# Performance work log

Hardware: AMD Instinct MI355X
Metric: run time of the kernel (lower is better)

Reference implementation:

```python
import jax, jax.numpy as jnp
import numpy as np

EMBED_DIM = 768
M, C = 8192, 4096
NEG_SAMPLES = 2   # args.neg_sample
CL_TEMP = 1.0
P_INF = 1000.0
EPS = 1e-8


def exp_map0(x, curv):
    # Lorentz exponential map at the origin (space components only, MERU-style).
    rc_xnorm = jnp.sqrt(curv) * jnp.linalg.norm(x, axis=-1, keepdims=True)
    return jnp.sinh(rc_xnorm) * x / jnp.maximum(rc_xnorm, EPS)


def pairwise_dist(x, y, curv):
    # x: (m, d) space components, y: (c, d); Lorentz geodesic distance.
    x_time = jnp.sqrt(1.0 / curv + jnp.sum(x * x, axis=-1))   # (m,)
    y_time = jnp.sqrt(1.0 / curv + jnp.sum(y * y, axis=-1))   # (c,)
    inner = x @ y.T - x_time[:, None] * y_time[None, :]        # Lorentz inner product (m, c)
    cd = jnp.maximum(-curv * inner, 1.0 + EPS)
    return jnp.arccosh(cd) / jnp.sqrt(curv)


def setup_inputs() -> dict:
    key = jax.random.key(0)
    k1, k2, k3 = jax.random.split(key, 3)
    return {
        "text_embeddings": jax.random.normal(k1, (M, EMBED_DIM), dtype=jnp.float32),
        "label_embeddings": jax.random.normal(k2, (C, EMBED_DIM), dtype=jnp.float32),
        "target_labels": jax.random.randint(k3, (M,), 0, C),
        "curv_log": jnp.float32(np.log(1.0)),                      # curv param (log-space)
        "text_alpha_log": jnp.float32(np.log(EMBED_DIM ** -0.5)),  # text_alpha (log-space)
        "label_alpha_log": jnp.float32(np.log(EMBED_DIM ** -0.5)), # label_alpha (log-space)
    }


def reference(text_embeddings, label_embeddings, target_labels, curv_log, text_alpha_log, label_alpha_log):
    curv = jnp.exp(curv_log)
    te = text_embeddings * jnp.exp(text_alpha_log)
    le = label_embeddings * jnp.exp(label_alpha_log)
    text_hyp = exp_map0(te, curv)
    label_hyp = exp_map0(le, curv)
    dist = pairwise_dist(text_hyp, label_hyp, curv)        # (m, c)
    m = dist.shape[0]
    rows = jnp.arange(m)
    # hard-negative mining: mask out the positive label, take k smallest distances
    masked = dist.at[rows, target_labels].set(P_INF)
    neg_minus_dist, _ = jax.lax.top_k(-masked, NEG_SAMPLES)  # (m, k) = -dist of hardest negatives
    neg_scores = neg_minus_dist / CL_TEMP                     # -dist / temp
    pos_score = -dist[rows, target_labels] / CL_TEMP          # (m,)
    denom = jnp.exp(pos_score) + jnp.sum(jnp.exp(neg_scores), axis=-1)
    loss = jnp.log(denom) - pos_score                         # = -log(exp(pos)/denom)
    return loss                                               # (m,) per-sample losses
```

## Files before the change

kernel.cpp:

```cpp
#include <hip/hip_runtime.h>
#include <hip/hip_bf16.h>
#include <math.h>

#define MM 8192
#define CC 4096
#define DD 768
#define EPSF 1e-8f

#define BM 256
#define BN 256
#define BK 64
#define TPB 512
#define NKT (DD / BK)
#define NROWT (MM / BM)
#define NCOLT (CC / BN)

#define XB_OFF 0
#define YB_OFF (MM * DD * 2)
#define FW_OFF (YB_OFF + CC * DD * 2)
#define S_T 0
#define T_T (MM)
#define S_L (2 * MM)
#define T_L (2 * MM + CC)
#define CA_T (2 * MM + 2 * CC)
#define POS  (CA_T + MM)
#define PART (POS + MM)

typedef __attribute__((ext_vector_type(8))) short short8;
typedef __attribute__((ext_vector_type(4))) unsigned short u16x4;
typedef __attribute__((ext_vector_type(4))) float f32x4;

__device__ inline unsigned short f2bf(float f) {
    unsigned int u = __float_as_uint(f);
    u += 0x7FFF + ((u >> 16) & 1);
    return (unsigned short)(u >> 16);
}

__device__ inline void gll16(const void* g, void* l) {
    __builtin_amdgcn_global_load_lds(
        (const __attribute__((address_space(1))) void*)(uintptr_t)g,
        (__attribute__((address_space(3))) void*)(unsigned)(uintptr_t)l,
        16, 0, 0);
}

#define BAR() do { __builtin_amdgcn_sched_barrier(0); __builtin_amdgcn_s_barrier(); __builtin_amdgcn_sched_barrier(0); } while (0)
#define VM8 asm volatile("s_waitcnt vmcnt(8)" ::: "memory")
#define VM4 asm volatile("s_waitcnt vmcnt(4)" ::: "memory")
#define VM0 asm volatile("s_waitcnt vmcnt(0)" ::: "memory")
#define NOPS ((void)0)

#define DSR(dst, base, off) \
    asm volatile("ds_read_b128 %0, %1 offset:%c2" : "=v"(dst) : "v"(base), "n"(off))

#define MFMA_B(a, b, c) __builtin_amdgcn_mfma_f32_16x16x32_bf16((a), (b), (c), 0, 0, 0)

__global__ void prep_conv_kernel(const float* __restrict__ X, const float* __restrict__ Y,
                                 const float* curv_log, const float* ta_log, const float* la_log,
                                 char* __restrict__ wsb) {
    unsigned short* Xb = (unsigned short*)(wsb + XB_OFF);
    unsigned short* Yb = (unsigned short*)(wsb + YB_OFF);
    float* fws = (float*)(wsb + FW_OFF);
    int wid = threadIdx.x >> 6, lane = threadIdx.x & 63;
    int row = blockIdx.x * 4 + wid;
    float curv = __expf(curv_log[0]);
    const float* src; unsigned short* dst; float alpha; int idx; int is_text;
    if (row < MM) {
        src = X + (size_t)row * DD; dst = Xb + (size_t)row * DD;
        alpha = __expf(ta_log[0]); idx = row; is_text = 1;
    } else {
        int r = row - MM;
        src = Y + (size_t)r * DD; dst = Yb + (size_t)r * DD;
        alpha = __expf(la_log[0]); idx = r; is_text = 0;
    }
    float n2 = 0.f;
    #pragma unroll
    for (int j = 0; j < 3; ++j) {
        float4 v = *(const float4*)(src + lane * 4 + 256 * j);
        n2 += v.x * v.x + v.y * v.y + v.z * v.z + v.w * v.w;
        u16x4 o; o[0] = f2bf(v.x); o[1] = f2bf(v.y); o[2] = f2bf(v.z); o[3] = f2bf(v.w);
        *(u16x4*)(dst + lane * 4 + 256 * j) = o;
    }
    #pragma unroll
    for (int m = 32; m; m >>= 1) n2 += __shfl_xor(n2, m);
    if (lane == 0) {
        float r = sqrtf(curv) * alpha * sqrtf(n2);
        float s = alpha * sinhf(r) / fmaxf(r, EPSF);
        float tt = sqrtf(1.0f / curv + s * s * n2);
        if (is_text) {
            fws[S_T + idx] = s; fws[T_T + idx] = tt; fws[CA_T + idx] = tt / s;
        } else {
            fws[S_L + idx] = s; fws[T_L + idx] = tt;
        }
    }
}

__global__ void pos_kernel(const float* __restrict__ X, const float* __restrict__ Y,
                           const int* __restrict__ tgt, const float* curv_log,
                           char* __restrict__ wsb) {
    float* fws = (float*)(wsb + FW_OFF);
    int wid = threadIdx.x >> 6, lane = threadIdx.x & 63;
    int row = blockIdx.x * 4 + wid;
    if (row >= MM) return;
    float curv = __expf(curv_log[0]);
    int t = tgt[row];
    const float* xr = X + (size_t)row * DD;
    const float* yr = Y + (size_t)t * DD;
    float dot = 0.f;
    #pragma unroll
    for (int k = 0; k < DD / 64; ++k) dot += xr[lane + 64 * k] * yr[lane + 64 * k];
    #pragma unroll
    for (int m = 32; m; m >>= 1) dot += __shfl_xor(dot, m);
    if (lane == 0) {
        float inner = fws[S_T + row] * fws[S_L + t] * dot - fws[T_T + row] * fws[T_L + t];
        float cd = fmaxf(-curv * inner, 1.0f + EPSF);
        float d = __logf(cd + sqrtf(cd * cd - 1.0f)) * rsqrtf(curv);
        fws[POS + row] = d;
    }
}

__global__ __launch_bounds__(TPB, 2) void main_kernel(
    const int* __restrict__ tgt, char* __restrict__ wsb)
{
    __shared__ unsigned short Ald[4 * 8192];
    __shared__ unsigned short Bld[4 * 8192];
    __shared__ float red[256][4][2];

    const unsigned short* Xb = (const unsigned short*)(wsb + XB_OFF);
    const unsigned short* Yb = (const unsigned short*)(wsb + YB_OFF);
    float* fws = (float*)(wsb + FW_OFF);

    int tid = threadIdx.x;
    int lane = tid & 63, wid = tid >> 6;
    int wr = wid >> 2, wc = wid & 3;
    int l15 = lane & 15, rgrp = lane >> 4;

    int bid = blockIdx.x;
    int pos = bid >> 3;
    int coltile = pos >> 2;
    int rowpanel = (bid & 7) * 4 + (pos & 3);
    int rowbase = rowpanel * BM;
    int colbase = coltile * BN;

    int ko_src = ((tid & 3) ^ ((tid >> 3) & 3)) * 8;
    const unsigned short* xk = Xb + (size_t)(rowbase + (tid >> 2)) * DD + ko_src;
    const unsigned short* yk = Yb + (size_t)(colbase + (tid >> 2)) * DD + ko_src;
    unsigned short* adst = Ald + tid * 8;
    unsigned short* bdst = Bld + tid * 8;

#define STG_A(OFF, RG) do { gll16(xk + (OFF), adst + (RG) * 8192); \
                            gll16(xk + (size_t)128 * DD + (OFF), adst + (RG) * 8192 + 4096); } while (0)
#define STG_B(OFF, RG) do { gll16(yk + (OFF), bdst + (RG) * 8192); \
                            gll16(yk + (size_t)128 * DD + (OFF), bdst + (RG) * 8192 + 4096); } while (0)

    unsigned a_base = (unsigned)(uintptr_t)(&Ald[0]) + (wr * 128 + l15) * 64
                      + ((rgrp * 16) ^ (((l15 >> 1) & 3) << 4));
    unsigned b_base = (unsigned)(uintptr_t)(&Bld[0]) + (wc * 64 + l15) * 64
                      + ((rgrp * 16) ^ (((l15 >> 1) & 3) << 4));

    f32x4 acc[8][4];
    #pragma unroll
    for (int a = 0; a < 8; ++a)
        #pragma unroll
        for (int b = 0; b < 4; ++b)
            acc[a][b] = (f32x4){0.f, 0.f, 0.f, 0.f};

    short8 af[4], bf[4];

#define MF16(AO) do { \
    acc[(AO)+0][0] = MFMA_B(af[0], bf[0], acc[(AO)+0][0]); \
    acc[(AO)+0][1] = MFMA_B(af[0], bf[1], acc[(AO)+0][1]); \
    acc[(AO)+0][2] = MFMA_B(af[0], bf[2], acc[(AO)+0][2]); \
    acc[(AO)+0][3] = MFMA_B(af[0], bf[3], acc[(AO)+0][3]); \
    acc[(AO)+1][0] = MFMA_B(af[1], bf[0], acc[(AO)+1][0]); \
    acc[(AO)+1][1] = MFMA_B(af[1], bf[1], acc[(AO)+1][1]); \
    acc[(AO)+1][2] = MFMA_B(af[1], bf[2], acc[(AO)+1][2]); \
    acc[(AO)+1][3] = MFMA_B(af[1], bf[3], acc[(AO)+1][3]); \
    acc[(AO)+2][0] = MFMA_B(af[2], bf[0], acc[(AO)+2][0]); \
    acc[(AO)+2][1] = MFMA_B(af[2], bf[1], acc[(AO)+2][1]); \
    acc[(AO)+2][2] = MFMA_B(af[2], bf[2], acc[(AO)+2][2]); \
    acc[(AO)+2][3] = MFMA_B(af[2], bf[3], acc[(AO)+2][3]); \
    acc[(AO)+3][0] = MFMA_B(af[3], bf[0], acc[(AO)+3][0]); \
    acc[(AO)+3][1] = MFMA_B(af[3], bf[1], acc[(AO)+3][1]); \
    acc[(AO)+3][2] = MFMA_B(af[3], bf[2], acc[(AO)+3][2]); \
    acc[(AO)+3][3] = MFMA_B(af[3], bf[3], acc[(AO)+3][3]); \
} while (0)

#define PHASE(RG, MH, AO, STG, W) do { \
    if ((MH) == 0) { \
        DSR(bf[0], b_base, (RG) * 16384 + 0); \
        DSR(bf[1], b_base, (RG) * 16384 + 1024); \
        DSR(bf[2], b_base, (RG) * 16384 + 2048); \
        DSR(bf[3], b_base, (RG) * 16384 + 3072); \
    } \
    DSR(af[0], a_base, (RG) * 16384 + ((MH) * 4 + 0) * 1024); \
    DSR(af[1], a_base, (RG) * 16384 + ((MH) * 4 + 1) * 1024); \
    DSR(af[2], a_base, (RG) * 16384 + ((MH) * 4 + 2) * 1024); \
    DSR(af[3], a_base, (RG) * 16384 + ((MH) * 4 + 3) * 1024); \
    STG; \
    W; \
    BAR(); \
    asm volatile("s_waitcnt lgkmcnt(0)" ::: "memory"); \
    __builtin_amdgcn_sched_barrier(0); \
    __builtin_amdgcn_s_setprio(1); \
    MF16(AO); \
    __builtin_amdgcn_s_setprio(0); \
    BAR(); \
} while (0)

    STG_A(0, 0);  STG_B(0, 0);
    STG_A(32, 1); STG_B(32, 1);
    STG_A(64, 2); STG_B(64, 2);
    VM8;
    BAR();

    #pragma unroll 1
    for (int kp = 0; kp < 5; ++kp) {
        PHASE(0, 0, 0, STG_A(96, 3),  NOPS);
        PHASE(0, 1, 4, STG_B(96, 3),  VM8);
        PHASE(1, 0, 0, STG_A(128, 0), NOPS);
        PHASE(1, 1, 4, STG_B(128, 0), VM8);
        PHASE(2, 0, 0, STG_A(160, 1), NOPS);
        PHASE(2, 1, 4, STG_B(160, 1), VM8);
        PHASE(3, 0, 0, STG_A(192, 2), NOPS);
        PHASE(3, 1, 4, STG_B(192, 2), VM8);
        xk += 128; yk += 128;
    }
    PHASE(0, 0, 0, STG_A(96, 3), NOPS);
    PHASE(0, 1, 4, STG_B(96, 3), VM8);
    PHASE(1, 0, 0, NOPS, NOPS);
    PHASE(1, 1, 4, NOPS, VM4);
    PHASE(2, 0, 0, NOPS, NOPS);
    PHASE(2, 1, 4, NOPS, VM0);
    PHASE(3, 0, 0, NOPS, NOPS);
    PHASE(3, 1, 4, NOPS, NOPS);

    int colb = colbase + wc * 64 + l15;
    float sbv[4], tbv[4];
    #pragma unroll
    for (int nf = 0; nf < 4; ++nf) { sbv[nf] = fws[S_L + colb + nf * 16]; tbv[nf] = fws[T_L + colb + nf * 16]; }

    float m1[32], m2[32];
    #pragma unroll
    for (int mf = 0; mf < 8; ++mf) {
        int rw = rowbase + wr * 128 + mf * 16 + rgrp * 4;
        #pragma unroll
        for (int j = 0; j < 4; ++j) {
            float ca = fws[CA_T + rw + j];
            int tgj = tgt[rw + j];
            float a = -3.4e38f, b = -3.4e38f;
            #pragma unroll
            for (int nf = 0; nf < 4; ++nf) {
                float u = sbv[nf] * acc[mf][nf][j] - ca * tbv[nf];
                if (colb + nf * 16 == tgj) u = -3.4e38f;
                float n1 = fmaxf(a, u);
                b = fmaxf(b, fminf(a, u));
                a = n1;
            }
            m1[mf * 4 + j] = a; m2[mf * 4 + j] = b;
        }
    }
    #pragma unroll
    for (int mask = 1; mask <= 8; mask <<= 1)
        #pragma unroll
        for (int i = 0; i < 32; ++i) {
            float o1 = __shfl_xor(m1[i], mask);
            float o2 = __shfl_xor(m2[i], mask);
            float n1 = fmaxf(m1[i], o1);
            m2[i] = fmaxf(fminf(m1[i], o1), fmaxf(m2[i], o2));
            m1[i] = n1;
        }
    if (l15 == 0) {
        #pragma unroll
        for (int mf = 0; mf < 8; ++mf)
            #pragma unroll
            for (int j = 0; j < 4; ++j) {
                int rl = wr * 128 + mf * 16 + rgrp * 4 + j;
                red[rl][wc][0] = m1[mf * 4 + j];
                red[rl][wc][1] = m2[mf * 4 + j];
            }
    }
    __syncthreads();
    if (tid < 256) {
        float p1 = -3.4e38f, p2 = -3.4e38f;
        #pragma unroll
        for (int g = 0; g < 4; ++g) {
            float a1 = red[tid][g][0], a2 = red[tid][g][1];
            float n1 = fmaxf(p1, a1);
            p2 = fmaxf(fminf(p1, a1), fmaxf(p2, a2));
            p1 = n1;
        }
        int row = rowbase + tid;
        fws[PART + ((size_t)row * NCOLT + coltile) * 2 + 0] = p1;
        fws[PART + ((size_t)row * NCOLT + coltile) * 2 + 1] = p2;
    }
}

__global__ void final_kernel(const char* __restrict__ wsb, const float* __restrict__ curv_log,
                             float* __restrict__ out) {
    const float* fws = (const float*)(wsb + FW_OFF);
    int row = blockIdx.x * 256 + threadIdx.x;
    if (row >= MM) return;
    float curv = __expf(curv_log[0]);
    float rsc = rsqrtf(curv);
    const float* p = fws + PART + (size_t)row * (NCOLT * 2);
    float p1 = -3.4e38f, p2 = -3.4e38f;
    #pragma unroll
    for (int s = 0; s < NCOLT; ++s) {
        float a1 = p[s * 2], a2 = p[s * 2 + 1];
        float n1 = fmaxf(p1, a1);
        p2 = fmaxf(fminf(p1, a1), fmaxf(p2, a2));
        p1 = n1;
    }
    float sa = fws[S_T + row];
    float i1 = sa * p1, i2 = sa * p2;
    float cd1 = fmaxf(-curv * i1, 1.0f + EPSF);
    float d1 = __logf(cd1 + sqrtf(cd1 * cd1 - 1.0f)) * rsc;
    float cd2 = fmaxf(-curv * i2, 1.0f + EPSF);
    float d2 = __logf(cd2 + sqrtf(cd2 * cd2 - 1.0f)) * rsc;
    float dp = fws[POS + row];
    float denom = __expf(-dp) + __expf(-d1) + __expf(-d2);
    out[row] = __logf(denom) + dp;
}

extern "C" void kernel_launch(void* const* d_in, const int* in_sizes, int n_in,
                              void* d_out, int out_size, void* d_ws, size_t ws_size,
                              hipStream_t stream) {
    const float* X = (const float*)d_in[0];
    const float* Y = (const float*)d_in[1];
    const int* tgt = (const int*)d_in[2];
    const float* curv_log = (const float*)d_in[3];
    const float* ta_log = (const float*)d_in[4];
    const float* la_log = (const float*)d_in[5];
    char* wsb = (char*)d_ws;
    float* out = (float*)d_out;

    prep_conv_kernel<<<(MM + CC) / 4, 256, 0, stream>>>(X, Y, curv_log, ta_log, la_log, wsb);
    pos_kernel<<<MM / 4, 256, 0, stream>>>(X, Y, tgt, curv_log, wsb);
    main_kernel<<<NROWT * NCOLT, TPB, 0, stream>>>(tgt, wsb);
    final_kernel<<<MM / 256, 256, 0, stream>>>(wsb, curv_log, out);
}
```

Measured before the change: 89.17 us.

## Double-buffer LDS fragment reads to overlap ds_read with MFMA in GEMM main loop

Splits the A and B register fragments into ping-pong buffers so each phase issues the LDS reads for the next sub-tile before running the MFMAs on the current one. It waits only partially on lgkmcnt and adjusts the vmcnt waits to match. It also drops the min-blocks-per-CU launch bound so the compiler can use more registers for the extra fragment buffers. This costs more VGPRs, which may lower occupancy, and relies on the hand-tuned waitcnt values staying correct.

```diff
diff --git a/kernel.cpp b/kernel.cpp
--- a/kernel.cpp
+++ b/kernel.cpp
@@ -45,6 +45,7 @@
 
 #define BAR() do { __builtin_amdgcn_sched_barrier(0); __builtin_amdgcn_s_barrier(); __builtin_amdgcn_sched_barrier(0); } while (0)
 #define VM8 asm volatile("s_waitcnt vmcnt(8)" ::: "memory")
+#define VM6 asm volatile("s_waitcnt vmcnt(6)" ::: "memory")
 #define VM4 asm volatile("s_waitcnt vmcnt(4)" ::: "memory")
 #define VM0 asm volatile("s_waitcnt vmcnt(0)" ::: "memory")
 #define NOPS ((void)0)
@@ -118,7 +119,7 @@
     }
 }
 
-__global__ __launch_bounds__(TPB, 2) void main_kernel(
+__global__ __launch_bounds__(TPB) void main_kernel(
     const int* __restrict__ tgt, char* __restrict__ wsb)
 {
     __shared__ unsigned short Ald[4 * 8192];
@@ -164,45 +165,47 @@
         for (int b = 0; b < 4; ++b)
             acc[a][b] = (f32x4){0.f, 0.f, 0.f, 0.f};
 
-    short8 af[4], bf[4];
-
-#define MF16(AO) do { \
-    acc[(AO)+0][0] = MFMA_B(af[0], bf[0], acc[(AO)+0][0]); \
-    acc[(AO)+0][1] = MFMA_B(af[0], bf[1], acc[(AO)+0][1]); \
-    acc[(AO)+0][2] = MFMA_B(af[0], bf[2], acc[(AO)+0][2]); \
-    acc[(AO)+0][3] = MFMA_B(af[0], bf[3], acc[(AO)+0][3]); \
-    acc[(AO)+1][0] = MFMA_B(af[1], bf[0], acc[(AO)+1][0]); \
-    acc[(AO)+1][1] = MFMA_B(af[1], bf[1], acc[(AO)+1][1]); \
-    acc[(AO)+1][2] = MFMA_B(af[1], bf[2], acc[(AO)+1][2]); \
-    acc[(AO)+1][3] = MFMA_B(af[1], bf[3], acc[(AO)+1][3]); \
-    acc[(AO)+2][0] = MFMA_B(af[2], bf[0], acc[(AO)+2][0]); \
-    acc[(AO)+2][1] = MFMA_B(af[2], bf[1], acc[(AO)+2][1]); \
-    acc[(AO)+2][2] = MFMA_B(af[2], bf[2], acc[(AO)+2][2]); \
-    acc[(AO)+2][3] = MFMA_B(af[2], bf[3], acc[(AO)+2][3]); \
-    acc[(AO)+3][0] = MFMA_B(af[3], bf[0], acc[(AO)+3][0]); \
-    acc[(AO)+3][1] = MFMA_B(af[3], bf[1], acc[(AO)+3][1]); \
-    acc[(AO)+3][2] = MFMA_B(af[3], bf[2], acc[(AO)+3][2]); \
-    acc[(AO)+3][3] = MFMA_B(af[3], bf[3], acc[(AO)+3][3]); \
+    short8 afE[4], afO[4], bf0[4], bf1[4];
+
+#define LDA(S, RG, MH) do { \
+    DSR(S[0], a_base, (RG) * 16384 + ((MH) * 4 + 0) * 1024); \
+    DSR(S[1], a_base, (RG) * 16384 + ((MH) * 4 + 1) * 1024); \
+    DSR(S[2], a_base, (RG) * 16384 + ((MH) * 4 + 2) * 1024); \
+    DSR(S[3], a_base, (RG) * 16384 + ((MH) * 4 + 3) * 1024); } while (0)
+#define LDB(S, RG) do { \
+    DSR(S[0], b_base, (RG) * 16384 + 0); \
+    DSR(S[1], b_base, (RG) * 16384 + 1024); \
+    DSR(S[2], b_base, (RG) * 16384 + 2048); \
+    DSR(S[3], b_base, (RG) * 16384 + 3072); } while (0)
+
+#define MF16(AF, BF, AO) do { \
+    acc[(AO)+0][0] = MFMA_B(AF[0], BF[0], acc[(AO)+0][0]); \
+    acc[(AO)+0][1] = MFMA_B(AF[0], BF[1], acc[(AO)+0][1]); \
+    acc[(AO)+0][2] = MFMA_B(AF[0], BF[2], acc[(AO)+0][2]); \
+    acc[(AO)+0][3] = MFMA_B(AF[0], BF[3], acc[(AO)+0][3]); \
+    acc[(AO)+1][0] = MFMA_B(AF[1], BF[0], acc[(AO)+1][0]); \
+    acc[(AO)+1][1] = MFMA_B(AF[1], BF[1], acc[(AO)+1][1]); \
+    acc[(AO)+1][2] = MFMA_B(AF[1], BF[2], acc[(AO)+1][2]); \
+    acc[(AO)+1][3] = MFMA_B(AF[1], BF[3], acc[(AO)+1][3]); \
+    acc[(AO)+2][0] = MFMA_B(AF[2], BF[0], acc[(AO)+2][0]); \
+    acc[(AO)+2][1] = MFMA_B(AF[2], BF[1], acc[(AO)+2][1]); \
+    acc[(AO)+2][2] = MFMA_B(AF[2], BF[2], acc[(AO)+2][2]); \
+    acc[(AO)+2][3] = MFMA_B(AF[2], BF[3], acc[(AO)+2][3]); \
+    acc[(AO)+3][0] = MFMA_B(AF[3], BF[0], acc[(AO)+3][0]); \
+    acc[(AO)+3][1] = MFMA_B(AF[3], BF[1], acc[(AO)+3][1]); \
+    acc[(AO)+3][2] = MFMA_B(AF[3], BF[2], acc[(AO)+3][2]); \
+    acc[(AO)+3][3] = MFMA_B(AF[3], BF[3], acc[(AO)+3][3]); \
 } while (0)
 
-#define PHASE(RG, MH, AO, STG, W) do { \
-    if ((MH) == 0) { \
-        DSR(bf[0], b_base, (RG) * 16384 + 0); \
-        DSR(bf[1], b_base, (RG) * 16384 + 1024); \
-        DSR(bf[2], b_base, (RG) * 16384 + 2048); \
-        DSR(bf[3], b_base, (RG) * 16384 + 3072); \
-    } \
-    DSR(af[0], a_base, (RG) * 16384 + ((MH) * 4 + 0) * 1024); \
-    DSR(af[1], a_base, (RG) * 16384 + ((MH) * 4 + 1) * 1024); \
-    DSR(af[2], a_base, (RG) * 16384 + ((MH) * 4 + 2) * 1024); \
-    DSR(af[3], a_base, (RG) * 16384 + ((MH) * 4 + 3) * 1024); \
+#define PH(LD, STG, W, LGN, MF) do { \
+    LD; \
     STG; \
     W; \
     BAR(); \
-    asm volatile("s_waitcnt lgkmcnt(0)" ::: "memory"); \
+    asm volatile("s_waitcnt lgkmcnt(" #LGN ")" ::: "memory"); \
     __builtin_amdgcn_sched_barrier(0); \
     __builtin_amdgcn_s_setprio(1); \
-    MF16(AO); \
+    MF; \
     __builtin_amdgcn_s_setprio(0); \
     BAR(); \
 } while (0)
@@ -212,27 +215,28 @@
     STG_A(64, 2); STG_B(64, 2);
     VM8;
     BAR();
+    LDB(bf0, 0); LDA(afE, 0, 0);
 
     #pragma unroll 1
     for (int kp = 0; kp < 5; ++kp) {
-        PHASE(0, 0, 0, STG_A(96, 3),  NOPS);
-        PHASE(0, 1, 4, STG_B(96, 3),  VM8);
-        PHASE(1, 0, 0, STG_A(128, 0), NOPS);
-        PHASE(1, 1, 4, STG_B(128, 0), VM8);
-        PHASE(2, 0, 0, STG_A(160, 1), NOPS);
-        PHASE(2, 1, 4, STG_B(160, 1), VM8);
-        PHASE(3, 0, 0, STG_A(192, 2), NOPS);
-        PHASE(3, 1, 4, STG_B(192, 2), VM8);
+        PH(LDA(afO, 0, 1),               STG_A(96, 3),  VM6, 4, MF16(afE, bf0, 0));
+        PH(LDB(bf1, 1); LDA(afE, 1, 0),  STG_B(96, 3),  VM6, 8, MF16(afO, bf0, 4));
+        PH(LDA(afO, 1, 1),               STG_A(128, 0), VM6, 4, MF16(afE, bf1, 0));
+        PH(LDB(bf0, 2); LDA(afE, 2, 0),  STG_B(128, 0), VM6, 8, MF16(afO, bf1, 4));
+        PH(LDA(afO, 2, 1),               STG_A(160, 1), VM6, 4, MF16(afE, bf0, 0));
+        PH(LDB(bf1, 3); LDA(afE, 3, 0),  STG_B(160, 1), VM6, 8, MF16(afO, bf0, 4));
+        PH(LDA(afO, 3, 1),               STG_A(192, 2), VM6, 4, MF16(afE, bf1, 0));
+        PH(LDB(bf0, 0); LDA(afE, 0, 0),  STG_B(192, 2), VM6, 8, MF16(afO, bf1, 4));
         xk += 128; yk += 128;
     }
-    PHASE(0, 0, 0, STG_A(96, 3), NOPS);
-    PHASE(0, 1, 4, STG_B(96, 3), VM8);
-    PHASE(1, 0, 0, NOPS, NOPS);
-    PHASE(1, 1, 4, NOPS, VM4);
-    PHASE(2, 0, 0, NOPS, NOPS);
-    PHASE(2, 1, 4, NOPS, VM0);
-    PHASE(3, 0, 0, NOPS, NOPS);
-    PHASE(3, 1, 4, NOPS, NOPS);
+    PH(LDA(afO, 0, 1),               STG_A(96, 3), VM6, 4, MF16(afE, bf0, 0));
+    PH(LDB(bf1, 1); LDA(afE, 1, 0),  STG_B(96, 3), VM6, 8, MF16(afO, bf0, 4));
+    PH(LDA(afO, 1, 1),               NOPS, VM4, 4, MF16(afE, bf1, 0));
+    PH(LDB(bf0, 2); LDA(afE, 2, 0),  NOPS, VM0, 8, MF16(afO, bf1, 4));
+    PH(LDA(afO, 2, 1),               NOPS, NOPS, 4, MF16(afE, bf0, 0));
+    PH(LDB(bf1, 3); LDA(afE, 3, 0),  NOPS, NOPS, 8, MF16(afO, bf0, 4));
+    PH(LDA(afO, 3, 1),               NOPS, NOPS, 4, MF16(afE, bf1, 0));
+    PH(NOPS,                         NOPS, NOPS, 0, MF16(afO, bf1, 4));
 
     int colb = colbase + wc * 64 + l15;
     float sbv[4], tbv[4];
```

New measurement: 88.58 us. About the same (-0.7%).
